# Performance work log

Measured on AMD Instinct MI355X. Metric: run time of the kernel, lower is better.

The kernel has to match this reference:

```python
import jax, jax.numpy as jnp
import numpy as np

D = 128      # d_model
H = 4        # n_heads
DH = D // H  # 32 head dim
TD = int(DH * 0.25)  # 8 time dims per head
T_DIM = TD * H       # 32 model-level time dims (MinkowskiLayerNorm t_dim)
EPS = 1e-5


def _ln(v, g, b):
    mu = jnp.mean(v, axis=-1, keepdims=True)
    var = jnp.mean(jnp.square(v - mu), axis=-1, keepdims=True)
    return (v - mu) * jax.lax.rsqrt(var + EPS) * g + b


def _minkowski_ln(x, gt, bt, gs, bs):
    # Normalize time-like and space-like coordinate blocks separately.
    return jnp.concatenate([_ln(x[..., :T_DIM], gt, bt), _ln(x[..., T_DIM:], gs, bs)], axis=-1)


def _lorentz_attn(x, Wq, bq, Wk, bk, Wv, bv, Wo, bo):
    B, S, _ = x.shape
    split = lambda y: y.reshape(B, S, H, DH).transpose(0, 2, 1, 3)  # [B,H,S,DH]
    q = split(x @ Wq + bq)
    k = split(x @ Wk + bk)
    v = split(x @ Wv + bv)
    # Minkowski metric signature (-,...,-,+,...,+): first TD dims of each head are time-like.
    eta = jnp.concatenate([-jnp.ones((TD,), x.dtype), jnp.ones((DH - TD,), x.dtype)])
    logits = jnp.einsum('bhqd,bhkd->bhqk', q * eta, k) / np.float32(np.sqrt(DH))
    w = jax.nn.softmax(logits, axis=-1)  # [B,H,S,S]
    o = jnp.einsum('bhqk,bhkd->bhqd', w, v).transpose(0, 2, 1, 3).reshape(B, S, D)
    return o @ Wo + bo


def setup_inputs() -> dict:
    key = jax.random.key(0)
    ks = jax.random.split(key, 8)
    s = 0.02
    inp = {
        'x': jax.random.normal(ks[0], (8, 2048, D), jnp.float32),
        'Wq': jax.random.normal(ks[1], (D, D), jnp.float32) * s,
        'bq': jnp.zeros((D,), jnp.float32),
        'Wk': jax.random.normal(ks[2], (D, D), jnp.float32) * s,
        'bk': jnp.zeros((D,), jnp.float32),
        'Wv': jax.random.normal(ks[3], (D, D), jnp.float32) * s,
        'bv': jnp.zeros((D,), jnp.float32),
        'Wo': jax.random.normal(ks[4], (D, D), jnp.float32) * s,
        'bo': jnp.zeros((D,), jnp.float32),
        'g1t': jnp.ones((T_DIM,), jnp.float32), 'b1t': jnp.zeros((T_DIM,), jnp.float32),
        'g1s': jnp.ones((D - T_DIM,), jnp.float32), 'b1s': jnp.zeros((D - T_DIM,), jnp.float32),
        'W1': jax.random.normal(ks[5], (D, 4 * D), jnp.float32) * s,
        'bf1': jnp.zeros((4 * D,), jnp.float32),
        'W2': jax.random.normal(ks[6], (4 * D, D), jnp.float32) * s,
        'bf2': jnp.zeros((D,), jnp.float32),
        'g2t': jnp.ones((T_DIM,), jnp.float32), 'b2t': jnp.zeros((T_DIM,), jnp.float32),
        'g2s': jnp.ones((D - T_DIM,), jnp.float32), 'b2s': jnp.zeros((D - T_DIM,), jnp.float32),
    }
    return inp


def reference(x, Wq, bq, Wk, bk, Wv, bv, Wo, bo,
              g1t, b1t, g1s, b1s, W1, bf1, W2, bf2,
              g2t, b2t, g2s, b2s):
    a = _lorentz_attn(x, Wq, bq, Wk, bk, Wv, bv, Wo, bo)
    x = _minkowski_ln(x + a, g1t, b1t, g1s, b1s)
    h = jax.nn.gelu(x @ W1 + bf1, approximate=False) @ W2 + bf2  # exact GELU (torch default)
    return _minkowski_ln(x + h, g2t, b2t, g2s, b2s)
```

## Files before the change

kernel.cpp:

```cpp
#include <hip/hip_runtime.h>
#include <hip/hip_bf16.h>

#define DEV __device__ __forceinline__

typedef __attribute__((ext_vector_type(8))) short short8;
typedef __attribute__((ext_vector_type(4))) float f32x4;

constexpr int D   = 128;
constexpr int S   = 2048;
constexpr int Hh  = 4;
constexpr int DH  = 32;
constexpr float QSCALE = 0.17677669529663687f * 1.4426950408889634f;
constexpr float EPSV = 1e-5f;

DEV unsigned short f2b(float f) {
  __hip_bfloat16 h = __float2bfloat16(f);
  return *reinterpret_cast<unsigned short*>(&h);
}
DEV unsigned pack2(float a, float b) {
  unsigned r;
  asm("v_cvt_pk_bf16_f32 %0, %1, %2" : "=v"(r) : "v"(a), "v"(b));
  return r;
}

DEV float fast_gelu(float v) {
  float z = v * 0.70710678118654752f;
  float a = fabsf(z);
  float t = __builtin_amdgcn_rcpf(1.0f + 0.3275911f * a);
  float p = t * (0.254829592f + t * (-0.284496736f +
            t * (1.421413741f + t * (-1.453152027f + t * 1.061405429f))));
  float e = __builtin_amdgcn_exp2f(-1.4426950408889634f * (z * z));
  float er = copysignf(1.0f - p * e, z);
  return 0.5f * v * (1.0f + er);
}


__global__ __launch_bounds__(256) void prep_kernel(
    const float* __restrict__ x,
    const float* __restrict__ Wq, const float* __restrict__ Wk,
    const float* __restrict__ Wv, const float* __restrict__ Wo,
    const float* __restrict__ W1, const float* __restrict__ W2,
    unsigned short* __restrict__ xb,
    unsigned short* __restrict__ wqT, unsigned short* __restrict__ wkT,
    unsigned short* __restrict__ wvT, unsigned short* __restrict__ woT,
    unsigned short* __restrict__ w1T, unsigned short* __restrict__ w2T) {
  int b = blockIdx.x, t = threadIdx.x;
  if (b < 1024) {
    int i8 = (b * 256 + t) * 8;
    int row = i8 >> 7, k0 = i8 & 127;
    const float4* p = reinterpret_cast<const float4*>(x + i8);
    float4 v0 = p[0], v1 = p[1];
    uint4 o;
    o.x = pack2(v0.x, v0.y);
    o.y = pack2(v0.z, v0.w);
    o.z = pack2(v1.x, v1.y);
    o.w = pack2(v1.z, v1.w);
    size_t off = ((size_t)(row >> 4) * 4 + (k0 >> 5)) * 512 + ((k0 & 31) >> 3) * 128 + (row & 15) * 8;
    *reinterpret_cast<uint4*>(xb + off) = o;
    return;
  }
  const float* src; unsigned short* dst; int nsh, KS, base;
  if      (b < 1088) { src = Wq; dst = wqT; nsh = 7; KS = 4;  base = 1024; }
  else if (b < 1152) { src = Wk; dst = wkT; nsh = 7; KS = 4;  base = 1088; }
  else if (b < 1216) { src = Wv; dst = wvT; nsh = 7; KS = 4;  base = 1152; }
  else if (b < 1280) { src = Wo; dst = woT; nsh = 7; KS = 4;  base = 1216; }
  else if (b < 1536) { src = W1; dst = w1T; nsh = 9; KS = 4;  base = 1280; }
  else               { src = W2; dst = w2T; nsh = 7; KS = 16; base = 1536; }
  int idx = (b - base) * 256 + t;
  int k = idx >> nsh, n = idx & ((1 << nsh) - 1);
  size_t off = ((size_t)(n >> 4) * KS + (k >> 5)) * 512 + ((k & 31) >> 3) * 128 + (n & 15) * 8 + (k & 7);
  dst[off] = f2b(src[idx]);
}

template <int KDIM, bool SWAP>
DEV void gemm_tile_fl(const unsigned short* __restrict__ A,
                      const unsigned short* __restrict__ BT,
                      int tileA, int tileB0, int lane, f32x4 acc[8]) {
  constexpr int KS = KDIM / 32;
#pragma unroll
  for (int ks = 0; ks < KS; ++ks) {
    short8 a = *reinterpret_cast<const short8*>(A + ((size_t)(tileA * KS + ks) * 64 + lane) * 8);
#pragma unroll
    for (int c = 0; c < 8; ++c) {
      short8 b = *reinterpret_cast<const short8*>(BT + ((size_t)((tileB0 + c) * KS + ks) * 64 + lane) * 8);
      if constexpr (SWAP)
        acc[c] = __builtin_amdgcn_mfma_f32_16x16x32_bf16(b, a, acc[c], 0, 0, 0);
      else
        acc[c] = __builtin_amdgcn_mfma_f32_16x16x32_bf16(a, b, acc[c], 0, 0, 0);
    }
  }
}

__global__ __launch_bounds__(256) void qkv_kernel(
    const unsigned short* __restrict__ xb,
    const unsigned short* __restrict__ wqT, const unsigned short* __restrict__ wkT,
    const unsigned short* __restrict__ wvT,
    const float* __restrict__ bq, const float* __restrict__ bk, const float* __restrict__ bv,
    unsigned short* __restrict__ q, unsigned short* __restrict__ k,
    unsigned short* __restrict__ vT) {
  int w = threadIdx.x >> 6, lane = threadIdx.x & 63;
  int g = lane >> 4, ln = lane & 15;
  int z = blockIdx.y;
  int row0 = blockIdx.x * 64 + w * 16;
  int tileA = blockIdx.x * 4 + w;
  const unsigned short* BT = (z == 0) ? wqT : (z == 1) ? wkT : wvT;
  const float* bias = (z == 0) ? bq : (z == 1) ? bk : bv;
  f32x4 acc[8];
#pragma unroll
  for (int c = 0; c < 8; ++c) acc[c] = f32x4{0.f, 0.f, 0.f, 0.f};
  if (z == 2) {
    gemm_tile_fl<128, false>(xb, BT, tileA, 0, lane, acc);
    int t0 = row0 + 4 * g;
    int b_ = t0 >> 11, s0 = t0 & 2047;
#pragma unroll
    for (int c = 0; c < 8; ++c) {
      int n = c * 16 + ln;
      int h = n >> 5, dh = n & 31;
      float bi = bias[n];
      size_t tile = ((size_t)(b_ * Hh + h) * 32 + (s0 >> 6)) * 4 + ((s0 & 63) >> 5) * 2 + (dh >> 4);
      size_t off = tile * 512 + ((s0 & 31) >> 3) * 128 + (dh & 15) * 8 + (s0 & 7);
      uint2 st;
      st.x = pack2(acc[c][0] + bi, acc[c][1] + bi);
      st.y = pack2(acc[c][2] + bi, acc[c][3] + bi);
      *reinterpret_cast<uint2*>(vT + off) = st;
    }
  } else {
    gemm_tile_fl<128, true>(xb, BT, tileA, 0, lane, acc);
    unsigned short* dst = (z == 0) ? q : k;
    int t = row0 + ln;
    int b_ = t >> 11, s = t & 2047;
#pragma unroll
    for (int c = 0; c < 8; ++c) {
      int nc = c * 16 + 4 * g;
      int h = nc >> 5, dh0 = nc & 31;
      f32x4 bi = *reinterpret_cast<const f32x4*>(bias + nc);
      float f = 1.0f;
      if (z == 0) f = (dh0 < 8) ? -QSCALE : QSCALE;
      float v0 = (acc[c][0] + bi[0]) * f, v1 = (acc[c][1] + bi[1]) * f;
      float v2 = (acc[c][2] + bi[2]) * f, v3 = (acc[c][3] + bi[3]) * f;
      size_t tile = (size_t)(b_ * Hh + h) * 128 + (s >> 4);
      size_t off = tile * 512 + ((dh0 >> 3) * 16 + (s & 15)) * 8 + (dh0 & 7);
      uint2 st;
      st.x = pack2(v0, v1);
      st.y = pack2(v2, v3);
      *reinterpret_cast<uint2*>(dst + off) = st;
    }
  }
}

__global__ __launch_bounds__(512, 4) void attn_kernel(
    const unsigned short* __restrict__ q, const unsigned short* __restrict__ k,
    const unsigned short* __restrict__ vT, unsigned short* __restrict__ ao) {
  __shared__ float smem_f[7680];
  int w = threadIdx.x >> 6, lane = threadIdx.x & 63;
  int g = lane >> 4, ln = lane & 15;
  int w_q = w >> 2, w_kv = w & 3;
  int bh = blockIdx.y;
  int qbase = blockIdx.x * 64 + w_q * 32;
  const unsigned short* qp = q + (size_t)bh * S * DH + lane * 8;
  const unsigned short* kp = k + (size_t)bh * S * DH + lane * 8;
  const unsigned short* vp = vT + (size_t)bh * DH * S + lane * 8;

  short8 qfr[2];
#pragma unroll
  for (int qf = 0; qf < 2; ++qf)
    qfr[qf] = *reinterpret_cast<const short8*>(qp + (size_t)((qbase >> 4) + qf) * 512);

  short8 ones;
#pragma unroll
  for (int j = 0; j < 8; ++j) ones[j] = (short)0x3F80;

  float m[2] = {0.f, 0.f};
  int mz[2] = {1, 1};
  f32x4 acc[2][2];
  f32x4 acc_l[2];
#pragma unroll
  for (int a = 0; a < 2; ++a) {
    acc_l[a] = f32x4{0.f, 0.f, 0.f, 0.f};
#pragma unroll
    for (int b = 0; b < 2; ++b) acc[a][b] = f32x4{0.f, 0.f, 0.f, 0.f};
  }

  short8 kf[4];
  {
    int kv0 = w_kv * 512;
#pragma unroll
    for (int c = 0; c < 4; ++c)
      kf[c] = *reinterpret_cast<const short8*>(kp + (size_t)((kv0 >> 4) + c) * 512);
  }

#pragma unroll 2
  for (int kt = 0; kt < 8; ++kt) {
    int kv0 = w_kv * 512 + kt * 64;
    short8 vfr[2][2];
#pragma unroll
    for (int hv = 0; hv < 2; ++hv)
#pragma unroll
      for (int vf = 0; vf < 2; ++vf)
        vfr[hv][vf] = *reinterpret_cast<const short8*>(vp + (size_t)((kv0 >> 6) * 4 + hv * 2 + vf) * 512);
    short8 kf_n[4];
    {
      int ktn = (kt < 7) ? kt + 1 : 7;
      int kvn = w_kv * 512 + ktn * 64;
#pragma unroll
      for (int c = 0; c < 4; ++c)
        kf_n[c] = *reinterpret_cast<const short8*>(kp + (size_t)((kvn >> 4) + c) * 512);
    }
    f32x4 sst[4][2];
#pragma unroll
    for (int c = 0; c < 4; ++c)
#pragma unroll
      for (int qf = 0; qf < 2; ++qf)
        sst[c][qf] = __builtin_amdgcn_mfma_f32_16x16x32_bf16(kf[c], qfr[qf],
                                                             f32x4{0.f, 0.f, 0.f, 0.f}, 0, 0, 0);
    short8 pfr[2][2];
#pragma unroll
    for (int qf = 0; qf < 2; ++qf) {
      if (__builtin_amdgcn_readfirstlane(mz[qf])) {
#pragma unroll
        for (int c = 0; c < 4; ++c)
#pragma unroll
          for (int r = 0; r < 4; ++r)
            sst[c][qf][r] = __builtin_amdgcn_exp2f(sst[c][qf][r]);
      } else {
#pragma unroll
        for (int c = 0; c < 4; ++c)
#pragma unroll
          for (int r = 0; r < 4; ++r)
            sst[c][qf][r] = __builtin_amdgcn_exp2f(sst[c][qf][r] - m[qf]);
      }
      unsigned Wc[4][2];
#pragma unroll
      for (int c = 0; c < 4; ++c) {
        Wc[c][0] = pack2(sst[c][qf][0], sst[c][qf][1]);
        Wc[c][1] = pack2(sst[c][qf][2], sst[c][qf][3]);
      }
#pragma unroll
      for (int hv = 0; hv < 2; ++hv) {
        unsigned f00, f01, f10, f11;
        {
          auto st = __builtin_amdgcn_permlane32_swap(Wc[2 * hv][0], Wc[2 * hv + 1][0], false, false);
          auto uv = __builtin_amdgcn_permlane16_swap(st[0], st[1], false, false);
          f00 = uv[0]; f10 = uv[1];
        }
        {
          auto st = __builtin_amdgcn_permlane32_swap(Wc[2 * hv][1], Wc[2 * hv + 1][1], false, false);
          auto uv = __builtin_amdgcn_permlane16_swap(st[0], st[1], false, false);
          f01 = uv[0]; f11 = uv[1];
        }
        union { unsigned u[4]; short8 s8; } pu;
        pu.u[0] = f00; pu.u[1] = f01; pu.u[2] = f10; pu.u[3] = f11;
        pfr[qf][hv] = pu.s8;
      }
    }
    __builtin_amdgcn_s_setprio(1);
#pragma unroll
    for (int hv = 0; hv < 2; ++hv) {
#pragma unroll
      for (int qf = 0; qf < 2; ++qf) {
#pragma unroll
        for (int vf = 0; vf < 2; ++vf)
          acc[vf][qf] = __builtin_amdgcn_mfma_f32_16x16x32_bf16(vfr[hv][vf], pfr[qf][hv], acc[vf][qf], 0, 0, 0);
        acc_l[qf] = __builtin_amdgcn_mfma_f32_16x16x32_bf16(ones, pfr[qf][hv], acc_l[qf], 0, 0, 0);
      }
    }
    __builtin_amdgcn_s_setprio(0);
#pragma unroll
    for (int qf = 0; qf < 2; ++qf) {
      float ls = acc_l[qf][0];
      if (!__all(ls <= 16777216.0f)) {
        float lg = __builtin_amdgcn_logf(ls);
        float cs = __builtin_amdgcn_rcpf(ls);
        m[qf] += lg;
        mz[qf] = 0;
#pragma unroll
        for (int vf = 0; vf < 2; ++vf)
#pragma unroll
          for (int r = 0; r < 4; ++r) acc[vf][qf][r] *= cs;
#pragma unroll
        for (int r = 0; r < 4; ++r) acc_l[qf][r] *= cs;
      }
    }
#pragma unroll
    for (int c = 0; c < 4; ++c) kf[c] = kf_n[c];
  }
  __syncthreads();
  if (w_kv) {
    float* mb = smem_f + ((w_q * 3 + (w_kv - 1)) * 64 + lane) * 20;
    mb[0] = m[0]; mb[1] = m[1]; mb[2] = acc_l[0][0]; mb[3] = acc_l[1][0];
#pragma unroll
    for (int vf = 0; vf < 2; ++vf)
#pragma unroll
      for (int qf = 0; qf < 2; ++qf)
#pragma unroll
        for (int r = 0; r < 4; ++r) mb[4 + (vf * 2 + qf) * 4 + r] = acc[vf][qf][r];
  }
  __syncthreads();
  if (w_kv == 0) {
    const float* mb0 = smem_f + ((w_q * 3 + 0) * 64 + lane) * 20;
    const float* mb1 = smem_f + ((w_q * 3 + 1) * 64 + lane) * 20;
    const float* mb2 = smem_f + ((w_q * 3 + 2) * 64 + lane) * 20;
    int b_ = bh >> 2, h = bh & 3;
#pragma unroll
    for (int qf = 0; qf < 2; ++qf) {
      float mt = fmaxf(fmaxf(m[qf], mb0[qf]), fmaxf(mb1[qf], mb2[qf]));
      float e0 = __builtin_amdgcn_exp2f(m[qf] - mt);
      float e1 = __builtin_amdgcn_exp2f(mb0[qf] - mt);
      float e2 = __builtin_amdgcn_exp2f(mb1[qf] - mt);
      float e3 = __builtin_amdgcn_exp2f(mb2[qf] - mt);
      float lt = acc_l[qf][0] * e0 + mb0[2 + qf] * e1 + mb1[2 + qf] * e2 + mb2[2 + qf] * e3;
      float inv = 1.0f / lt;
      int qrow = qbase + qf * 16 + ln;
#pragma unroll
      for (int vf = 0; vf < 2; ++vf) {
        int kk = h * 32 + vf * 16 + 4 * g;
        float o[4];
        int ai = 4 + (vf * 2 + qf) * 4;
#pragma unroll
        for (int r = 0; r < 4; ++r)
          o[r] = (acc[vf][qf][r] * e0 + mb0[ai + r] * e1 + mb1[ai + r] * e2 + mb2[ai + r] * e3) * inv;
        uint2 st;
        st.x = pack2(o[0], o[1]);
        st.y = pack2(o[2], o[3]);
        size_t grow = (size_t)b_ * S + qrow;
        size_t off = ((grow >> 4) * 4 + (kk >> 5)) * 512 + ((kk & 31) >> 3) * 128 + (grow & 15) * 8 + (kk & 7);
        *reinterpret_cast<uint2*>(ao + off) = st;
      }
    }
  }
}

__global__ __launch_bounds__(512) void tail_kernel(
    const unsigned short* __restrict__ ao, const unsigned short* __restrict__ woT,
    const float* __restrict__ bo, const float* __restrict__ x,
    const float* __restrict__ g1t, const float* __restrict__ b1t,
    const float* __restrict__ g1s, const float* __restrict__ b1s,
    const unsigned short* __restrict__ w1T, const float* __restrict__ bf1,
    const unsigned short* __restrict__ w2T, const float* __restrict__ bf2,
    const float* __restrict__ g2t, const float* __restrict__ b2t,
    const float* __restrict__ g2s, const float* __restrict__ b2s,
    float* __restrict__ out) {
  __shared__ unsigned short xbl[32][136];
  __shared__ unsigned short hl[32][520];
  __shared__ float stats[2][4][16][2];
  int w = threadIdx.x >> 6, lane = threadIdx.x & 63;
  int wm = w & 1, wn = w >> 1;
  int g = lane >> 4, ln = lane & 15;
  int row = blockIdx.x * 32 + wm * 16 + ln;
  int lrow = wm * 16 + ln;

  f32x4 acc1[2];
  acc1[0] = f32x4{0.f, 0.f, 0.f, 0.f};
  acc1[1] = f32x4{0.f, 0.f, 0.f, 0.f};
#pragma unroll
  for (int ks = 0; ks < 4; ++ks) {
    short8 a = *reinterpret_cast<const short8*>(ao + ((size_t)((blockIdx.x * 2 + wm) * 4 + ks) * 64 + lane) * 8);
#pragma unroll
    for (int c2 = 0; c2 < 2; ++c2) {
      short8 b = *reinterpret_cast<const short8*>(woT + ((size_t)((wn * 2 + c2) * 4 + ks) * 64 + lane) * 8);
      acc1[c2] = __builtin_amdgcn_mfma_f32_16x16x32_bf16(b, a, acc1[c2], 0, 0, 0);
    }
  }
  float rv[2][4];
  {
    float sum = 0.f, sq = 0.f;
#pragma unroll
    for (int c2 = 0; c2 < 2; ++c2) {
      int nc = wn * 32 + c2 * 16 + 4 * g;
      f32x4 bi = *reinterpret_cast<const f32x4*>(bo + nc);
      f32x4 xr = *reinterpret_cast<const f32x4*>(x + (size_t)row * D + nc);
#pragma unroll
      for (int r = 0; r < 4; ++r) {
        float v = acc1[c2][r] + bi[r] + xr[r];
        rv[c2][r] = v;
        sum += v; sq += v * v;
      }
    }
    sum += __shfl_xor(sum, 16); sum += __shfl_xor(sum, 32);
    sq  += __shfl_xor(sq, 16);  sq  += __shfl_xor(sq, 32);
    stats[wm][wn][ln][0] = sum;
    stats[wm][wn][ln][1] = sq;
  }
  __syncthreads();
  f32x4 xv[2];
  {
    float mu, rs;
    if (wn == 0) {
      float s = stats[wm][0][ln][0], q2 = stats[wm][0][ln][1];
      mu = s * (1.f / 32.f);
      rs = rsqrtf(q2 * (1.f / 32.f) - mu * mu + EPSV);
    } else {
      float s  = stats[wm][1][ln][0] + stats[wm][2][ln][0] + stats[wm][3][ln][0];
      float q2 = stats[wm][1][ln][1] + stats[wm][2][ln][1] + stats[wm][3][ln][1];
      mu = s * (1.f / 96.f);
      rs = rsqrtf(q2 * (1.f / 96.f) - mu * mu + EPSV);
    }
#pragma unroll
    for (int c2 = 0; c2 < 2; ++c2) {
      int nc = wn * 32 + c2 * 16 + 4 * g;
      f32x4 ga, bb;
      if (wn == 0) { ga = *reinterpret_cast<const f32x4*>(g1t + nc);
                     bb = *reinterpret_cast<const f32x4*>(b1t + nc); }
      else         { ga = *reinterpret_cast<const f32x4*>(g1s + nc - 32);
                     bb = *reinterpret_cast<const f32x4*>(b1s + nc - 32); }
#pragma unroll
      for (int r = 0; r < 4; ++r)
        xv[c2][r] = (rv[c2][r] - mu) * rs * ga[r] + bb[r];
      uint2 sb;
      sb.x = pack2(xv[c2][0], xv[c2][1]);
      sb.y = pack2(xv[c2][2], xv[c2][3]);
      *reinterpret_cast<uint2*>(&xbl[lrow][nc]) = sb;
    }
  }
  __syncthreads();

  {
    f32x4 acc2[8];
#pragma unroll
    for (int c = 0; c < 8; ++c) acc2[c] = f32x4{0.f, 0.f, 0.f, 0.f};
#pragma unroll
    for (int ks = 0; ks < 4; ++ks) {
      short8 a = *reinterpret_cast<const short8*>(&xbl[lrow][ks * 32 + 8 * g]);
#pragma unroll
      for (int c = 0; c < 8; ++c) {
        short8 b = *reinterpret_cast<const short8*>(w1T + ((size_t)((wn * 8 + c) * 4 + ks) * 64 + lane) * 8);
        acc2[c] = __builtin_amdgcn_mfma_f32_16x16x32_bf16(b, a, acc2[c], 0, 0, 0);
      }
    }
#pragma unroll
    for (int c = 0; c < 8; ++c) {
      int nc = wn * 128 + c * 16 + 4 * g;
      f32x4 bi = *reinterpret_cast<const f32x4*>(bf1 + nc);
      float ge[4];
#pragma unroll
      for (int r = 0; r < 4; ++r)
        ge[r] = fast_gelu(acc2[c][r] + bi[r]);
      uint2 stv;
      stv.x = pack2(ge[0], ge[1]);
      stv.y = pack2(ge[2], ge[3]);
      *reinterpret_cast<uint2*>(&hl[lrow][nc]) = stv;
    }
  }
  __syncthreads();

  f32x4 acc3[2];
  acc3[0] = f32x4{0.f, 0.f, 0.f, 0.f};
  acc3[1] = f32x4{0.f, 0.f, 0.f, 0.f};
#pragma unroll
  for (int ks = 0; ks < 16; ++ks) {
    short8 a = *reinterpret_cast<const short8*>(&hl[lrow][ks * 32 + 8 * g]);
#pragma unroll
    for (int c2 = 0; c2 < 2; ++c2) {
      short8 b = *reinterpret_cast<const short8*>(w2T + ((size_t)((wn * 2 + c2) * 16 + ks) * 64 + lane) * 8);
      acc3[c2] = __builtin_amdgcn_mfma_f32_16x16x32_bf16(b, a, acc3[c2], 0, 0, 0);
    }
  }
  float rv2[2][4];
  {
    float sum = 0.f, sq = 0.f;
#pragma unroll
    for (int c2 = 0; c2 < 2; ++c2) {
      int nc = wn * 32 + c2 * 16 + 4 * g;
      f32x4 bi = *reinterpret_cast<const f32x4*>(bf2 + nc);
#pragma unroll
      for (int r = 0; r < 4; ++r) {
        float v = acc3[c2][r] + bi[r] + xv[c2][r];
        rv2[c2][r] = v;
        sum += v; sq += v * v;
      }
    }
    sum += __shfl_xor(sum, 16); sum += __shfl_xor(sum, 32);
    sq  += __shfl_xor(sq, 16);  sq  += __shfl_xor(sq, 32);
    stats[wm][wn][ln][0] = sum;
    stats[wm][wn][ln][1] = sq;
  }
  __syncthreads();
  {
    float mu, rs;
    if (wn == 0) {
      float s = stats[wm][0][ln][0], q2 = stats[wm][0][ln][1];
      mu = s * (1.f / 32.f);
      rs = rsqrtf(q2 * (1.f / 32.f) - mu * mu + EPSV);
    } else {
      float s  = stats[wm][1][ln][0] + stats[wm][2][ln][0] + stats[wm][3][ln][0];
      float q2 = stats[wm][1][ln][1] + stats[wm][2][ln][1] + stats[wm][3][ln][1];
      mu = s * (1.f / 96.f);
      rs = rsqrtf(q2 * (1.f / 96.f) - mu * mu + EPSV);
    }
#pragma unroll
    for (int c2 = 0; c2 < 2; ++c2) {
      int nc = wn * 32 + c2 * 16 + 4 * g;
      f32x4 ga, bb;
      if (wn == 0) { ga = *reinterpret_cast<const f32x4*>(g2t + nc);
                     bb = *reinterpret_cast<const f32x4*>(b2t + nc); }
      else         { ga = *reinterpret_cast<const f32x4*>(g2s + nc - 32);
                     bb = *reinterpret_cast<const f32x4*>(b2s + nc - 32); }
      f32x4 o4;
#pragma unroll
      for (int r = 0; r < 4; ++r)
        o4[r] = (rv2[c2][r] - mu) * rs * ga[r] + bb[r];
      *reinterpret_cast<f32x4*>(out + (size_t)row * D + nc) = o4;
    }
  }
}

extern "C" void kernel_launch(void* const* d_in, const int* in_sizes, int n_in,
                              void* d_out, int out_size, void* d_ws, size_t ws_size,
                              hipStream_t stream) {
  (void)in_sizes; (void)n_in; (void)out_size; (void)ws_size;
  const float* x   = (const float*)d_in[0];
  const float* Wq  = (const float*)d_in[1];
  const float* bq  = (const float*)d_in[2];
  const float* Wk  = (const float*)d_in[3];
  const float* bk  = (const float*)d_in[4];
  const float* Wv  = (const float*)d_in[5];
  const float* bv  = (const float*)d_in[6];
  const float* Wo  = (const float*)d_in[7];
  const float* bo  = (const float*)d_in[8];
  const float* g1t = (const float*)d_in[9];
  const float* b1t = (const float*)d_in[10];
  const float* g1s = (const float*)d_in[11];
  const float* b1s = (const float*)d_in[12];
  const float* W1  = (const float*)d_in[13];
  const float* bf1 = (const float*)d_in[14];
  const float* W2  = (const float*)d_in[15];
  const float* bf2 = (const float*)d_in[16];
  const float* g2t = (const float*)d_in[17];
  const float* b2t = (const float*)d_in[18];
  const float* g2s = (const float*)d_in[19];
  const float* b2s = (const float*)d_in[20];

  char* ws = (char*)d_ws;
  unsigned short* xb  = (unsigned short*)(ws);
  unsigned short* wqT = (unsigned short*)(ws + 4194304);
  unsigned short* wkT = wqT + 16384;
  unsigned short* wvT = wkT + 16384;
  unsigned short* woT = wvT + 16384;
  unsigned short* w1T = woT + 16384;
  unsigned short* w2T = w1T + 65536;
  unsigned short* qb  = w2T + 65536;
  unsigned short* kb  = qb + 2097152;
  unsigned short* vT  = kb + 2097152;
  unsigned short* ao  = vT + 2097152;
  float* outp = (float*)d_out;

  prep_kernel<<<1792, 256, 0, stream>>>(x, Wq, Wk, Wv, Wo, W1, W2,
                                        xb, wqT, wkT, wvT, woT, w1T, w2T);
  qkv_kernel<<<dim3(256, 3), 256, 0, stream>>>(xb, wqT, wkT, wvT, bq, bk, bv, qb, kb, vT);
  attn_kernel<<<dim3(32, 32), 512, 0, stream>>>(qb, kb, vT, ao);
  tail_kernel<<<512, 512, 0, stream>>>(ao, woT, bo, x, g1t, b1t, g1s, b1s,
                                       w1T, bf1, w2T, bf2, g2t, b2t, g2s, b2s, outp);
}
```

Measured before the change: 63.49 us.

## Repartition tail kernel warps across columns so each weight fragment serves both row groups

```diff
diff --git a/kernel.cpp b/kernel.cpp
--- a/kernel.cpp
+++ b/kernel.cpp
@@ -342,103 +342,110 @@
     float* __restrict__ out) {
   __shared__ unsigned short xbl[32][136];
   __shared__ unsigned short hl[32][520];
-  __shared__ float stats[2][4][16][2];
-  int w = threadIdx.x >> 6, lane = threadIdx.x & 63;
-  int wm = w & 1, wn = w >> 1;
+  __shared__ float stats[2][8][16][2];
+  int wn = threadIdx.x >> 6, lane = threadIdx.x & 63;
   int g = lane >> 4, ln = lane & 15;
-  int row = blockIdx.x * 32 + wm * 16 + ln;
-  int lrow = wm * 16 + ln;
+  int nc = wn * 16 + 4 * g;
 
   f32x4 acc1[2];
   acc1[0] = f32x4{0.f, 0.f, 0.f, 0.f};
   acc1[1] = f32x4{0.f, 0.f, 0.f, 0.f};
 #pragma unroll
   for (int ks = 0; ks < 4; ++ks) {
-    short8 a = *reinterpret_cast<const short8*>(ao + ((size_t)((blockIdx.x * 2 + wm) * 4 + ks) * 64 + lane) * 8);
-#pragma unroll
-    for (int c2 = 0; c2 < 2; ++c2) {
-      short8 b = *reinterpret_cast<const short8*>(woT + ((size_t)((wn * 2 + c2) * 4 + ks) * 64 + lane) * 8);
-      acc1[c2] = __builtin_amdgcn_mfma_f32_16x16x32_bf16(b, a, acc1[c2], 0, 0, 0);
+    short8 b = *reinterpret_cast<const short8*>(woT + ((size_t)(wn * 4 + ks) * 64 + lane) * 8);
+#pragma unroll
+    for (int rg = 0; rg < 2; ++rg) {
+      short8 a = *reinterpret_cast<const short8*>(ao + ((size_t)((blockIdx.x * 2 + rg) * 4 + ks) * 64 + lane) * 8);
+      acc1[rg] = __builtin_amdgcn_mfma_f32_16x16x32_bf16(b, a, acc1[rg], 0, 0, 0);
     }
   }
   float rv[2][4];
   {
-    float sum = 0.f, sq = 0.f;
-#pragma unroll
-    for (int c2 = 0; c2 < 2; ++c2) {
-      int nc = wn * 32 + c2 * 16 + 4 * g;
-      f32x4 bi = *reinterpret_cast<const f32x4*>(bo + nc);
+    f32x4 bi = *reinterpret_cast<const f32x4*>(bo + nc);
+#pragma unroll
+    for (int rg = 0; rg < 2; ++rg) {
+      int row = blockIdx.x * 32 + rg * 16 + ln;
       f32x4 xr = *reinterpret_cast<const f32x4*>(x + (size_t)row * D + nc);
+      float sum = 0.f, sq = 0.f;
 #pragma unroll
       for (int r = 0; r < 4; ++r) {
-        float v = acc1[c2][r] + bi[r] + xr[r];
-        rv[c2][r] = v;
+        float v = acc1[rg][r] + bi[r] + xr[r];
+        rv[rg][r] = v;
         sum += v; sq += v * v;
       }
-    }
-    sum += __shfl_xor(sum, 16); sum += __shfl_xor(sum, 32);
-    sq  += __shfl_xor(sq, 16);  sq  += __shfl_xor(sq, 32);
-    stats[wm][wn][ln][0] = sum;
-    stats[wm][wn][ln][1] = sq;
+      sum += __shfl_xor(sum, 16); sum += __shfl_xor(sum, 32);
+      sq  += __shfl_xor(sq, 16);  sq  += __shfl_xor(sq, 32);
+      stats[rg][wn][ln][0] = sum;
+      stats[rg][wn][ln][1] = sq;
+    }
   }
   __syncthreads();
   f32x4 xv[2];
   {
-    float mu, rs;
-    if (wn == 0) {
-      float s = stats[wm][0][ln][0], q2 = stats[wm][0][ln][1];
-      mu = s * (1.f / 32.f);
-      rs = rsqrtf(q2 * (1.f / 32.f) - mu * mu + EPSV);
-    } else {
-      float s  = stats[wm][1][ln][0] + stats[wm][2][ln][0] + stats[wm][3][ln][0];
-      float q2 = stats[wm][1][ln][1] + stats[wm][2][ln][1] + stats[wm][3][ln][1];
-      mu = s * (1.f / 96.f);
-      rs = rsqrtf(q2 * (1.f / 96.f) - mu * mu + EPSV);
-    }
-#pragma unroll
-    for (int c2 = 0; c2 < 2; ++c2) {
-      int nc = wn * 32 + c2 * 16 + 4 * g;
-      f32x4 ga, bb;
-      if (wn == 0) { ga = *reinterpret_cast<const f32x4*>(g1t + nc);
-                     bb = *reinterpret_cast<const f32x4*>(b1t + nc); }
-      else         { ga = *reinterpret_cast<const f32x4*>(g1s + nc - 32);
-                     bb = *reinterpret_cast<const f32x4*>(b1s + nc - 32); }
+    f32x4 ga, bb;
+    if (wn < 2) { ga = *reinterpret_cast<const f32x4*>(g1t + nc);
+                  bb = *reinterpret_cast<const f32x4*>(b1t + nc); }
+    else        { ga = *reinterpret_cast<const f32x4*>(g1s + nc - 32);
+                  bb = *reinterpret_cast<const f32x4*>(b1s + nc - 32); }
+#pragma unroll
+    for (int rg = 0; rg < 2; ++rg) {
+      float mu, rs;
+      if (wn < 2) {
+        float s  = stats[rg][0][ln][0] + stats[rg][1][ln][0];
+        float q2 = stats[rg][0][ln][1] + stats[rg][1][ln][1];
+        mu = s * (1.f / 32.f);
+        rs = rsqrtf(q2 * (1.f / 32.f) - mu * mu + EPSV);
+      } else {
+        float s  = stats[rg][2][ln][0] + stats[rg][3][ln][0] + stats[rg][4][ln][0]
+                 + stats[rg][5][ln][0] + stats[rg][6][ln][0] + stats[rg][7][ln][0];
+        float q2 = stats[rg][2][ln][1] + stats[rg][3][ln][1] + stats[rg][4][ln][1]
+                 + stats[rg][5][ln][1] + stats[rg][6][ln][1] + stats[rg][7][ln][1];
+        mu = s * (1.f / 96.f);
+        rs = rsqrtf(q2 * (1.f / 96.f) - mu * mu + EPSV);
+      }
 #pragma unroll
       for (int r = 0; r < 4; ++r)
-        xv[c2][r] = (rv[c2][r] - mu) * rs * ga[r] + bb[r];
+        xv[rg][r] = (rv[rg][r] - mu) * rs * ga[r] + bb[r];
       uint2 sb;
-      sb.x = pack2(xv[c2][0], xv[c2][1]);
-      sb.y = pack2(xv[c2][2], xv[c2][3]);
-      *reinterpret_cast<uint2*>(&xbl[lrow][nc]) = sb;
+      sb.x = pack2(xv[rg][0], xv[rg][1]);
+      sb.y = pack2(xv[rg][2], xv[rg][3]);
+      *reinterpret_cast<uint2*>(&xbl[rg * 16 + ln][nc]) = sb;
     }
   }
   __syncthreads();
 
   {
-    f32x4 acc2[8];
-#pragma unroll
-    for (int c = 0; c < 8; ++c) acc2[c] = f32x4{0.f, 0.f, 0.f, 0.f};
+    f32x4 acc2[2][4];
+#pragma unroll
+    for (int rg = 0; rg < 2; ++rg)
+#pragma unroll
+      for (int c = 0; c < 4; ++c) acc2[rg][c] = f32x4{0.f, 0.f, 0.f, 0.f};
 #pragma unroll
     for (int ks = 0; ks < 4; ++ks) {
-      short8 a = *reinterpret_cast<const short8*>(&xbl[lrow][ks * 32 + 8 * g]);
-#pragma unroll
-      for (int c = 0; c < 8; ++c) {
-        short8 b = *reinterpret_cast<const short8*>(w1T + ((size_t)((wn * 8 + c) * 4 + ks) * 64 + lane) * 8);
-        acc2[c] = __builtin_amdgcn_mfma_f32_16x16x32_bf16(b, a, acc2[c], 0, 0, 0);
-      }
-    }
-#pragma unroll
-    for (int c = 0; c < 8; ++c) {
-      int nc = wn * 128 + c * 16 + 4 * g;
-      f32x4 bi = *reinterpret_cast<const f32x4*>(bf1 + nc);
-      float ge[4];
-#pragma unroll
-      for (int r = 0; r < 4; ++r)
-        ge[r] = fast_gelu(acc2[c][r] + bi[r]);
-      uint2 stv;
-      stv.x = pack2(ge[0], ge[1]);
-      stv.y = pack2(ge[2], ge[3]);
-      *reinterpret_cast<uint2*>(&hl[lrow][nc]) = stv;
+      short8 a0 = *reinterpret_cast<const short8*>(&xbl[ln][ks * 32 + 8 * g]);
+      short8 a1 = *reinterpret_cast<const short8*>(&xbl[16 + ln][ks * 32 + 8 * g]);
+#pragma unroll
+      for (int c = 0; c < 4; ++c) {
+        short8 b = *reinterpret_cast<const short8*>(w1T + ((size_t)((wn * 4 + c) * 4 + ks) * 64 + lane) * 8);
+        acc2[0][c] = __builtin_amdgcn_mfma_f32_16x16x32_bf16(b, a0, acc2[0][c], 0, 0, 0);
+        acc2[1][c] = __builtin_amdgcn_mfma_f32_16x16x32_bf16(b, a1, acc2[1][c], 0, 0, 0);
+      }
+    }
+#pragma unroll
+    for (int c = 0; c < 4; ++c) {
+      int hc = wn * 64 + c * 16 + 4 * g;
+      f32x4 bi = *reinterpret_cast<const f32x4*>(bf1 + hc);
+#pragma unroll
+      for (int rg = 0; rg < 2; ++rg) {
+        float ge[4];
+#pragma unroll
+        for (int r = 0; r < 4; ++r)
+          ge[r] = fast_gelu(acc2[rg][c][r] + bi[r]);
+        uint2 stv;
+        stv.x = pack2(ge[0], ge[1]);
+        stv.y = pack2(ge[2], ge[3]);
+        *reinterpret_cast<uint2*>(&hl[rg * 16 + ln][hc]) = stv;
+      }
     }
   }
   __syncthreads();
@@ -448,57 +455,58 @@
   acc3[1] = f32x4{0.f, 0.f, 0.f, 0.f};
 #pragma unroll
   for (int ks = 0; ks < 16; ++ks) {
-    short8 a = *reinterpret_cast<const short8*>(&hl[lrow][ks * 32 + 8 * g]);
-#pragma unroll
-    for (int c2 = 0; c2 < 2; ++c2) {
-      short8 b = *reinterpret_cast<const short8*>(w2T + ((size_t)((wn * 2 + c2) * 16 + ks) * 64 + lane) * 8);
-      acc3[c2] = __builtin_amdgcn_mfma_f32_16x16x32_bf16(b, a, acc3[c2], 0, 0, 0);
-    }
+    short8 b = *reinterpret_cast<const short8*>(w2T + ((size_t)(wn * 16 + ks) * 64 + lane) * 8);
+    short8 a0 = *reinterpret_cast<const short8*>(&hl[ln][ks * 32 + 8 * g]);
+    short8 a1 = *reinterpret_cast<const short8*>(&hl[16 + ln][ks * 32 + 8 * g]);
+    acc3[0] = __builtin_amdgcn_mfma_f32_16x16x32_bf16(b, a0, acc3[0], 0, 0, 0);
+    acc3[1] = __builtin_amdgcn_mfma_f32_16x16x32_bf16(b, a1, acc3[1], 0, 0, 0);
   }
   float rv2[2][4];
   {
-    float sum = 0.f, sq = 0.f;
-#pragma unroll
-    for (int c2 = 0; c2 < 2; ++c2) {
-      int nc = wn * 32 + c2 * 16 + 4 * g;
-      f32x4 bi = *reinterpret_cast<const f32x4*>(bf2 + nc);
+    f32x4 bi = *reinterpret_cast<const f32x4*>(bf2 + nc);
+#pragma unroll
+    for (int rg = 0; rg < 2; ++rg) {
+      float sum = 0.f, sq = 0.f;
 #pragma unroll
       for (int r = 0; r < 4; ++r) {
-        float v = acc3[c2][r] + bi[r] + xv[c2][r];
-        rv2[c2][r] = v;
+        float v = acc3[rg][r] + bi[r] + xv[rg][r];
+        rv2[rg][r] = v;
         sum += v; sq += v * v;
       }
-    }
-    sum += __shfl_xor(sum, 16); sum += __shfl_xor(sum, 32);
-    sq  += __shfl_xor(sq, 16);  sq  += __shfl_xor(sq, 32);
-    stats[wm][wn][ln][0] = sum;
-    stats[wm][wn][ln][1] = sq;
+      sum += __shfl_xor(sum, 16); sum += __shfl_xor(sum, 32);
+      sq  += __shfl_xor(sq, 16);  sq  += __shfl_xor(sq, 32);
+      stats[rg][wn][ln][0] = sum;
+      stats[rg][wn][ln][1] = sq;
+    }
   }
   __syncthreads();
   {
-    float mu, rs;
-    if (wn == 0) {
-      float s = stats[wm][0][ln][0], q2 = stats[wm][0][ln][1];
-      mu = s * (1.f / 32.f);
-      rs = rsqrtf(q2 * (1.f / 32.f) - mu * mu + EPSV);
-    } else {
-      float s  = stats[wm][1][ln][0] + stats[wm][2][ln][0] + stats[wm][3][ln][0];
-      float q2 = stats[wm][1][ln][1] + stats[wm][2][ln][1] + stats[wm][3][ln][1];
-      mu = s * (1.f / 96.f);
-      rs = rsqrtf(q2 * (1.f / 96.f) - mu * mu + EPSV);
-    }
-#pragma unroll
-    for (int c2 = 0; c2 < 2; ++c2) {
-      int nc = wn * 32 + c2 * 16 + 4 * g;
-      f32x4 ga, bb;
-      if (wn == 0) { ga = *reinterpret_cast<const f32x4*>(g2t + nc);
-                     bb = *reinterpret_cast<const f32x4*>(b2t + nc); }
-      else         { ga = *reinterpret_cast<const f32x4*>(g2s + nc - 32);
-                     bb = *reinterpret_cast<const f32x4*>(b2s + nc - 32); }
+    f32x4 ga, bb;
+    if (wn < 2) { ga = *reinterpret_cast<const f32x4*>(g2t + nc);
+                  bb = *reinterpret_cast<const f32x4*>(b2t + nc); }
+    else        { ga = *reinterpret_cast<const f32x4*>(g2s + nc - 32);
+                  bb = *reinterpret_cast<const f32x4*>(b2s + nc - 32); }
+#pragma unroll
+    for (int rg = 0; rg < 2; ++rg) {
+      float mu, rs;
+      if (wn < 2) {
+        float s  = stats[rg][0][ln][0] + stats[rg][1][ln][0];
+        float q2 = stats[rg][0][ln][1] + stats[rg][1][ln][1];
+        mu = s * (1.f / 32.f);
+        rs = rsqrtf(q2 * (1.f / 32.f) - mu * mu + EPSV);
+      } else {
+        float s  = stats[rg][2][ln][0] + stats[rg][3][ln][0] + stats[rg][4][ln][0]
+                 + stats[rg][5][ln][0] + stats[rg][6][ln][0] + stats[rg][7][ln][0];
+        float q2 = stats[rg][2][ln][1] + stats[rg][3][ln][1] + stats[rg][4][ln][1]
+                 + stats[rg][5][ln][1] + stats[rg][6][ln][1] + stats[rg][7][ln][1];
+        mu = s * (1.f / 96.f);
+        rs = rsqrtf(q2 * (1.f / 96.f) - mu * mu + EPSV);
+      }
+      int row = blockIdx.x * 32 + rg * 16 + ln;
       f32x4 o4;
 #pragma unroll
       for (int r = 0; r < 4; ++r)
-        o4[r] = (rv2[c2][r] - mu) * rs * ga[r] + bb[r];
+        o4[r] = (rv2[rg][r] - mu) * rs * ga[r] + bb[r];
       *reinterpret_cast<f32x4*>(out + (size_t)row * D + nc) = o4;
     }
   }
```

After: 62.33 us. No clear change (-1.8%).
